# Kernel optimization log

Hardware: AMD Instinct MI355X
Metric: run time of the kernel (lower is better)

## Reference

```python
import jax, jax.numpy as jnp
import numpy as np

B, S, HID = 2, 1024, 2048
NH, NKV = 32, 8
HD = HID // NH          # 64
N_REP = NH // NKV       # 4
ROPE_BASE = 10000.0


def rope_tables(seq_len, dim):
    inv_freq = 1.0 / (ROPE_BASE ** (np.arange(0, dim, 2, dtype=np.float32) / dim))
    t = jnp.arange(seq_len, dtype=jnp.float32)
    freqs = jnp.outer(t, jnp.asarray(inv_freq))          # [S, HD/2]
    emb = jnp.concatenate([freqs, freqs], axis=-1)       # [S, HD]
    return jnp.cos(emb), jnp.sin(emb)


def rotate_half(x):
    half = x.shape[-1] // 2
    return jnp.concatenate([-x[..., half:], x[..., :half]], axis=-1)


def setup_inputs() -> dict:
    key = jax.random.key(0)
    k1, k2, k3, k4, k5 = jax.random.split(key, 5)
    hidden_states = jax.random.normal(k1, (B, S, HID), dtype=jnp.float32)
    position_ids = jnp.broadcast_to(jnp.arange(S, dtype=jnp.int32), (B, S))
    # additive causal mask [B,1,S,S]: 0 where allowed, large negative where masked
    neg = jnp.finfo(jnp.float32).min
    causal = jnp.tril(jnp.ones((S, S), dtype=bool))
    attention_mask = jnp.where(causal, 0.0, neg)[None, None].astype(jnp.float32)
    attention_mask = jnp.broadcast_to(attention_mask, (B, 1, S, S))
    scale = 0.02
    Wq = jax.random.normal(k2, (HID, NH * HD), dtype=jnp.float32) * scale
    Wk = jax.random.normal(k3, (HID, NKV * HD), dtype=jnp.float32) * scale
    Wv = jax.random.normal(k4, (HID, NKV * HD), dtype=jnp.float32) * scale
    Wo = jax.random.normal(k5, (HID, HID), dtype=jnp.float32) * scale
    return {"hidden_states": hidden_states, "position_ids": position_ids,
            "attention_mask": attention_mask, "Wq": Wq, "Wk": Wk, "Wv": Wv, "Wo": Wo}


def reference(hidden_states, position_ids, attention_mask, Wq, Wk, Wv, Wo):
    b, s, _ = hidden_states.shape
    q = (hidden_states @ Wq).reshape(b, s, NH, HD).transpose(0, 2, 1, 3)    # [b,H,s,d]
    k = (hidden_states @ Wk).reshape(b, s, NKV, HD).transpose(0, 2, 1, 3)   # [b,kv,s,d]
    v = (hidden_states @ Wv).reshape(b, s, NKV, HD).transpose(0, 2, 1, 3)

    cos_t, sin_t = rope_tables(s, HD)                    # [s, d]
    cos = cos_t[position_ids][:, None]                   # [b,1,s,d]
    sin = sin_t[position_ids][:, None]
    q = q * cos + rotate_half(q) * sin
    k = k * cos + rotate_half(k) * sin

    # GQA: repeat each kv head N_REP times along the head axis
    k = jnp.repeat(k, N_REP, axis=1)                     # [b,H,s,d]
    v = jnp.repeat(v, N_REP, axis=1)

    scale = 1.0 / jnp.sqrt(jnp.asarray(HD, dtype=q.dtype))
    scores = jnp.einsum('bhqd,bhkd->bhqk', q, k) * scale
    scores = scores + attention_mask
    scores = jnp.maximum(scores, jnp.finfo(scores.dtype).min)
    w = jax.nn.softmax(scores, axis=-1)
    out = jnp.einsum('bhqk,bhkd->bhqd', w, v)            # [b,H,s,d]
    out = out.transpose(0, 2, 1, 3).reshape(b, s, HID)
    return out @ Wo
```

## Files before the change

### kernel.cpp

```cpp
#include <hip/hip_runtime.h>
#include <hip/hip_bf16.h>
#include <math.h>

constexpr int BB   = 2;
constexpr int SS   = 1024;
constexpr int HID  = 2048;
constexpr int NH   = 32;
constexpr int NKV  = 8;
constexpr int HD   = 64;
constexpr int M    = BB * SS;
constexpr int NQKV = 3072;

typedef __attribute__((ext_vector_type(8))) short bf8v;
typedef __attribute__((ext_vector_type(4))) float f4v;

static __device__ __forceinline__ unsigned short f2b(float x) {
  __hip_bfloat16 h = __float2bfloat16(x);
  return *reinterpret_cast<unsigned short*>(&h);
}
static __device__ __forceinline__ void gload16(void* lds, const void* g) {
  __builtin_amdgcn_global_load_lds(
      (const __attribute__((address_space(1))) void*)g,
      (__attribute__((address_space(3))) void*)lds, 16, 0, 0);
}

__global__ __launch_bounds__(256) void prepAll(
    const float* __restrict__ Wq, const float* __restrict__ Wk,
    const float* __restrict__ Wv, const float* __restrict__ Wo,
    const float* __restrict__ hidden, const int* __restrict__ pos_ids,
    unsigned short* __restrict__ WqkvT, unsigned short* __restrict__ WoT,
    unsigned short* __restrict__ Xb, float2* __restrict__ tab) {
  const int z = blockIdx.z;
  const int t = threadIdx.x;

  if (z == 4) {
    const int idx = blockIdx.y * 32 + blockIdx.x;
    if ((t & 127) < 32) {
      const int m = idx * 2 + (t >> 7);
      const int j = t & 31;
      const float pos = (float)pos_ids[m];
      const float ang = pos * exp2f(-(float)j * (13.287712379549449f / 32.0f));
      float sn, cs;
      sincosf(ang, &sn, &cs);
      tab[(size_t)m * 32 + j] = make_float2(cs, sn);
    }
    return;
  }
  if (z == 5) {
    const size_t base = ((size_t)(blockIdx.y * 32 + blockIdx.x)) * 4096;
#pragma unroll
    for (int it = 0; it < 2; ++it) {
      const size_t i = base + it * 2048 + t * 8;
      const float4 v0 = *(const float4*)(hidden + i);
      const float4 v1 = *(const float4*)(hidden + i + 4);
      unsigned short o[8] = {f2b(v0.x), f2b(v0.y), f2b(v0.z), f2b(v0.w),
                             f2b(v1.x), f2b(v1.y), f2b(v1.z), f2b(v1.w)};
      *(bf8v*)(Xb + i) = *(bf8v*)o;
    }
    return;
  }

  const float* src;
  unsigned short* dst;
  int C;
  if (z == 0)      { src = Wq; dst = WqkvT;                      C = 2048; }
  else if (z == 1) { src = Wk; dst = WqkvT + (size_t)2048 * HID; C = 512;  }
  else if (z == 2) { src = Wv; dst = WqkvT + (size_t)2560 * HID; C = 512;  }
  else             { src = Wo; dst = WoT;                        C = 2048; }

  const int r0 = blockIdx.y * 64, c0 = blockIdx.x * 64;
  if (c0 >= C) return;
  __shared__ float T[64][65];
  {
    const int r  = t >> 2;
    const int c4 = (t & 3) * 16;
    const float* sp = src + (size_t)(r0 + r) * C + c0 + c4;
    *(float4*)&T[r][c4 + 0]  = *(const float4*)(sp + 0);
    *(float4*)&T[r][c4 + 4]  = *(const float4*)(sp + 4);
    *(float4*)&T[r][c4 + 8]  = *(const float4*)(sp + 8);
    *(float4*)&T[r][c4 + 12] = *(const float4*)(sp + 12);
  }
  __syncthreads();
  {
    const int c  = t >> 2;
    const int rr = (t & 3) * 16;
    unsigned short o[16];
#pragma unroll
    for (int i = 0; i < 16; ++i) o[i] = f2b(T[rr + i][c]);
    unsigned short* dp = dst + (size_t)(c0 + c) * HID + r0 + rr;
    *(bf8v*)dp       = *(bf8v*)&o[0];
    *(bf8v*)(dp + 8) = *(bf8v*)&o[8];
  }
}


__global__ __launch_bounds__(256) void gemm_qkv(
    const unsigned short* __restrict__ A, const unsigned short* __restrict__ Bt,
    const float2* __restrict__ tab,
    unsigned short* __restrict__ Qb, unsigned short* __restrict__ Kb,
    unsigned short* __restrict__ Vb) {
  __shared__ unsigned short As[4][64 * 32];
  __shared__ unsigned short Bs[4][128 * 32];
  const int t  = threadIdx.x;
  const int w  = t >> 6, l = t & 63;
  const int lr = l & 15, lg = l >> 4;
  const int wr = w >> 1, wc = w & 1;
  const int bm = blockIdx.y * 64, bn = blockIdx.x * 128;

  f4v acc[2][4] = {};

  const unsigned short* Ablk = A  + (size_t)bm * HID;
  const unsigned short* Bblk = Bt + (size_t)bn * HID;
  const int srow = l >> 2;
  const int scol = (((l & 3) ^ ((srow >> 1) & 3)) * 8);
  const int rsl  = (lg ^ ((lr >> 1) & 3)) * 8;

  auto stage = [&](int buf, int k0) {
    gload16(&As[buf][(w * 16) * 32], Ablk + (size_t)(w * 16 + srow) * HID + k0 + scol);
    gload16(&Bs[buf][(w * 32)      * 32], Bblk + (size_t)(w * 32 +      srow) * HID + k0 + scol);
    gload16(&Bs[buf][(w * 32 + 16) * 32], Bblk + (size_t)(w * 32 + 16 + srow) * HID + k0 + scol);
  };

  const int nsteps = HID / 32;
  stage(0, 0);
  stage(1, 32);
  stage(2, 64);
  asm volatile("s_waitcnt vmcnt(6)" ::: "memory");
  __builtin_amdgcn_s_barrier();

  const int aoff = (wr * 32 + lr) * 32 + rsl;
  const int boff = (wc * 64 + lr) * 32 + rsl;
  for (int tt = 0; tt < nsteps; ++tt) {
    const int cur = tt & 3;
    if (tt + 3 < nsteps) stage((tt + 3) & 3, (tt + 3) * 32);

    bf8v aF[2], bF[4];
#pragma unroll
    for (int i = 0; i < 2; ++i)
      aF[i] = *(const bf8v*)&As[cur][aoff + i * 512];
#pragma unroll
    for (int j = 0; j < 4; ++j)
      bF[j] = *(const bf8v*)&Bs[cur][boff + j * 512];
    __builtin_amdgcn_s_setprio(1);
#pragma unroll
    for (int mi = 0; mi < 2; ++mi)
#pragma unroll
      for (int ni = 0; ni < 4; ++ni)
        acc[mi][ni] = __builtin_amdgcn_mfma_f32_16x16x32_bf16(aF[mi], bF[ni], acc[mi][ni], 0, 0, 0);
    __builtin_amdgcn_s_setprio(0);

    if (tt + 3 < nsteps)      { asm volatile("s_waitcnt vmcnt(6)" ::: "memory"); }
    else if (tt + 2 < nsteps) { asm volatile("s_waitcnt vmcnt(3)" ::: "memory"); }
    else                      { asm volatile("s_waitcnt vmcnt(0)" ::: "memory"); }
    __builtin_amdgcn_s_barrier();
  }

  const int row0 = bm + wr * 32;
  const int colHead = bn + wc * 64;
  unsigned short* outArr;
  int hh, headsPerB, mode;
  if (colHead < 2048)      { mode = 0; outArr = Qb; hh = colHead >> 6;          headsPerB = NH;  }
  else if (colHead < 2560) { mode = 1; outArr = Kb; hh = (colHead - 2048) >> 6; headsPerB = NKV; }
  else                     { mode = 2; outArr = Vb; hh = (colHead - 2560) >> 6; headsPerB = NKV; }

#pragma unroll
  for (int mi = 0; mi < 2; ++mi)
#pragma unroll
    for (int r = 0; r < 4; ++r) {
      const int rowg = row0 + mi * 16 + lg * 4 + r;
      const int bI = rowg >> 10, s = rowg & (SS - 1);
      unsigned short* dst =
          outArr + ((size_t)(bI * headsPerB + hh) * SS + s) * 64;
      if (mode == 2) {
#pragma unroll
        for (int ni = 0; ni < 4; ++ni)
          dst[ni * 16 + lr] = f2b(acc[mi][ni][r]);
      } else {
        const float2 cs_lo = tab[(size_t)rowg * 32 + lr];
        const float2 cs_hi = tab[(size_t)rowg * 32 + 16 + lr];
#pragma unroll
        for (int ni = 0; ni < 4; ++ni) {
          const float2 cs = (ni & 1) ? cs_hi : cs_lo;
          const float x   = acc[mi][ni][r];
          const float prt = acc[mi][ni ^ 2][r];
          const float rh  = (ni < 2) ? -prt : prt;
          float v = x * cs.x + rh * cs.y;
          if (mode == 0) v *= 0.125f;
          dst[ni * 16 + lr] = f2b(v);
        }
      }
    }
}

__global__ __launch_bounds__(256) void gemm_bf16(
    const unsigned short* __restrict__ A, const unsigned short* __restrict__ Bt,
    float* __restrict__ C, int Ndim) {
  __shared__ unsigned short As[4][64 * 32];
  __shared__ unsigned short Bs[4][128 * 32];
  const int t  = threadIdx.x;
  const int w  = t >> 6, l = t & 63;
  const int lr = l & 15, lg = l >> 4;
  const int wr = w >> 1, wc = w & 1;
  const int bm = blockIdx.y * 64, bn = blockIdx.x * 128;

  f4v acc[2][4] = {};

  const unsigned short* Ablk = A  + (size_t)bm * HID;
  const unsigned short* Bblk = Bt + (size_t)bn * HID;
  const int srow = l >> 2;
  const int scol = (((l & 3) ^ ((srow >> 1) & 3)) * 8);
  const int rsl  = (lg ^ ((lr >> 1) & 3)) * 8;

  auto stage = [&](int buf, int k0) {
    gload16(&As[buf][(w * 16) * 32], Ablk + (size_t)(w * 16 + srow) * HID + k0 + scol);
    gload16(&Bs[buf][(w * 32)      * 32], Bblk + (size_t)(w * 32 +      srow) * HID + k0 + scol);
    gload16(&Bs[buf][(w * 32 + 16) * 32], Bblk + (size_t)(w * 32 + 16 + srow) * HID + k0 + scol);
  };

  const int nsteps = HID / 32;
  stage(0, 0);
  stage(1, 32);
  stage(2, 64);
  asm volatile("s_waitcnt vmcnt(6)" ::: "memory");
  __builtin_amdgcn_s_barrier();

  const int aoff = (wr * 32 + lr) * 32 + rsl;
  const int boff = (wc * 64 + lr) * 32 + rsl;
  for (int tt = 0; tt < nsteps; ++tt) {
    const int cur = tt & 3;
    if (tt + 3 < nsteps) stage((tt + 3) & 3, (tt + 3) * 32);

    bf8v aF[2], bF[4];
#pragma unroll
    for (int i = 0; i < 2; ++i)
      aF[i] = *(const bf8v*)&As[cur][aoff + i * 512];
#pragma unroll
    for (int j = 0; j < 4; ++j)
      bF[j] = *(const bf8v*)&Bs[cur][boff + j * 512];
    __builtin_amdgcn_s_setprio(1);
#pragma unroll
    for (int mi = 0; mi < 2; ++mi)
#pragma unroll
      for (int ni = 0; ni < 4; ++ni)
        acc[mi][ni] = __builtin_amdgcn_mfma_f32_16x16x32_bf16(aF[mi], bF[ni], acc[mi][ni], 0, 0, 0);
    __builtin_amdgcn_s_setprio(0);

    if (tt + 3 < nsteps)      { asm volatile("s_waitcnt vmcnt(6)" ::: "memory"); }
    else if (tt + 2 < nsteps) { asm volatile("s_waitcnt vmcnt(3)" ::: "memory"); }
    else                      { asm volatile("s_waitcnt vmcnt(0)" ::: "memory"); }
    __builtin_amdgcn_s_barrier();
  }

  const int row0 = bm + wr * 32;
  const int col0 = bn + wc * 64;
#pragma unroll
  for (int mi = 0; mi < 2; ++mi)
#pragma unroll
    for (int r = 0; r < 4; ++r) {
      const size_t rowoff = (size_t)(row0 + mi * 16 + lg * 4 + r) * Ndim;
#pragma unroll
      for (int ni = 0; ni < 4; ++ni)
        C[rowoff + col0 + ni * 16 + lr] = acc[mi][ni][r];
    }
}

__global__ __launch_bounds__(256) void vtrans(
    const unsigned short* __restrict__ Vb, unsigned short* __restrict__ Vt) {
  const int bkv = blockIdx.y;
  const int s0  = blockIdx.x * 64;
  __shared__ unsigned short T[64][72];
  const int t = threadIdx.x;
  const unsigned short* src = Vb + ((size_t)bkv * SS + s0) * 64;
  {
    const int r  = t >> 2;
    const int co = (t & 3) * 16;
    *(bf8v*)&T[r][co]     = *(const bf8v*)(src + (size_t)r * 64 + co);
    *(bf8v*)&T[r][co + 8] = *(const bf8v*)(src + (size_t)r * 64 + co + 8);
  }
  __syncthreads();
  {
    const int d  = t >> 2;
    const int so = (t & 3) * 16;
    unsigned short tmp[16];
#pragma unroll
    for (int i = 0; i < 16; ++i) tmp[i] = T[so + i][d];
    unsigned short* dst = Vt + ((size_t)(bkv * 64 + d)) * SS + s0 + so;
    *(bf8v*)dst       = *(bf8v*)&tmp[0];
    *(bf8v*)(dst + 8) = *(bf8v*)&tmp[8];
  }
}

__global__ __launch_bounds__(128) void attn_mfma(
    const unsigned short* __restrict__ Qb, const unsigned short* __restrict__ Kb,
    const unsigned short* __restrict__ Vt, unsigned short* __restrict__ attn) {
  const int xb = blockIdx.x;
  const int h = blockIdx.y, b = blockIdx.z;
  const int kv = h >> 2;
  const int w  = threadIdx.x >> 6;
  const int l  = threadIdx.x & 63;
  const int lr = l & 15;
  const int lg = l >> 4;
  const int t  = threadIdx.x;

  __shared__ unsigned short VT[64][72];
  __shared__ unsigned short PL[2][16][72];

  const unsigned short* Kp = Kb + ((size_t)((b * NKV + kv) * SS)) * 64;
  const unsigned short* Vp = Vt + ((size_t)((b * NKV + kv) * 64)) * SS;

  const int vd  = t >> 1;
  const int vso = (t & 1) * 32;

  for (int half = 0; half < 2; ++half) {
    const int qt = half ? (31 - xb) : xb;
    const int qbase = qt * 32;
    const int qW = qbase + w * 16;
    const unsigned short* Qp = Qb + ((size_t)((b * NH + h) * SS + qW)) * 64;
    bf8v aQ0 = *(const bf8v*)(Qp + (size_t)lr * 64 + lg * 8);
    bf8v aQ1 = *(const bf8v*)(Qp + (size_t)lr * 64 + 32 + lg * 8);

    f4v o[4] = {{0,0,0,0},{0,0,0,0},{0,0,0,0},{0,0,0,0}};
    float lsumL[4] = {0.f, 0.f, 0.f, 0.f};

    for (int kvb = 0; kvb < qbase + 32; kvb += 64) {
      __syncthreads();
      const unsigned short* vp = Vp + (size_t)vd * SS + kvb + vso;
      const bf8v v0 = *(const bf8v*)(vp);
      const bf8v v1 = *(const bf8v*)(vp + 8);
      const bf8v v2 = *(const bf8v*)(vp + 16);
      const bf8v v3 = *(const bf8v*)(vp + 24);

      f4v sc[4] = {{0,0,0,0},{0,0,0,0},{0,0,0,0},{0,0,0,0}};
      __builtin_amdgcn_s_setprio(1);
#pragma unroll
      for (int c = 0; c < 4; ++c) {
        const unsigned short* kr = Kp + (size_t)(kvb + c * 16 + lr) * 64 + lg * 8;
        bf8v b0 = *(const bf8v*)(kr);
        bf8v b1 = *(const bf8v*)(kr + 32);
        sc[c] = __builtin_amdgcn_mfma_f32_16x16x32_bf16(aQ0, b0, sc[c], 0, 0, 0);
        sc[c] = __builtin_amdgcn_mfma_f32_16x16x32_bf16(aQ1, b1, sc[c], 0, 0, 0);
      }
      __builtin_amdgcn_s_setprio(0);

#pragma unroll
      for (int r = 0; r < 4; ++r) {
        const int qrow = qW + lg * 4 + r;
        float ps = 0.f;
        unsigned short pb[4];
#pragma unroll
        for (int c = 0; c < 4; ++c) {
          const float s = ((kvb + c * 16 + lr) > qrow) ? -INFINITY : sc[c][r];
          const float p = __expf(s);
          ps += p;
          pb[c] = f2b(p);
        }
        lsumL[r] += ps;
#pragma unroll
        for (int c = 0; c < 4; ++c) PL[w][lg * 4 + r][c * 16 + lr] = pb[c];
      }

      *(bf8v*)&VT[vd][vso]      = v0;
      *(bf8v*)&VT[vd][vso + 8]  = v1;
      *(bf8v*)&VT[vd][vso + 16] = v2;
      *(bf8v*)&VT[vd][vso + 24] = v3;

      __syncthreads();

      bf8v aP0 = *(const bf8v*)&PL[w][lr][lg * 8];
      bf8v aP1 = *(const bf8v*)&PL[w][lr][32 + lg * 8];
      __builtin_amdgcn_s_setprio(1);
#pragma unroll
      for (int n = 0; n < 4; ++n) {
        bf8v bV0 = *(const bf8v*)&VT[n * 16 + lr][lg * 8];
        bf8v bV1 = *(const bf8v*)&VT[n * 16 + lr][32 + lg * 8];
        o[n] = __builtin_amdgcn_mfma_f32_16x16x32_bf16(aP0, bV0, o[n], 0, 0, 0);
        o[n] = __builtin_amdgcn_mfma_f32_16x16x32_bf16(aP1, bV1, o[n], 0, 0, 0);
      }
      __builtin_amdgcn_s_setprio(0);
    }

#pragma unroll
    for (int r = 0; r < 4; ++r) {
      float ls = lsumL[r];
      ls += __shfl_xor(ls, 1);
      ls += __shfl_xor(ls, 2);
      ls += __shfl_xor(ls, 4);
      ls += __shfl_xor(ls, 8);
      const float inv = 1.0f / ls;
      const int row = qW + lg * 4 + r;
      unsigned short* dst = attn + (size_t)(b * SS + row) * HID + h * 64;
#pragma unroll
      for (int n = 0; n < 4; ++n) dst[n * 16 + lr] = f2b(o[n][r] * inv);
    }
  }
}

extern "C" void kernel_launch(void* const* d_in, const int* in_sizes, int n_in,
                              void* d_out, int out_size, void* d_ws, size_t ws_size,
                              hipStream_t stream) {
  const float* hidden = (const float*)d_in[0];
  const int*   pos    = (const int*)d_in[1];
  const float* Wq = (const float*)d_in[3];
  const float* Wk = (const float*)d_in[4];
  const float* Wv = (const float*)d_in[5];
  const float* Wo = (const float*)d_in[6];
  float* out = (float*)d_out;

  char* ws = (char*)d_ws;
  unsigned short* WqkvT = (unsigned short*)(ws);
  unsigned short* WoT   = (unsigned short*)(ws + 12582912);
  unsigned short* Xb    = (unsigned short*)(ws + 20971520);
  unsigned short* attnb = Xb;
  unsigned short* Qb    = (unsigned short*)(ws + 29360128);
  unsigned short* Kb    = (unsigned short*)(ws + 37748736);
  unsigned short* Vb    = (unsigned short*)(ws + 39845888);
  unsigned short* Vt    = (unsigned short*)(ws + 41943040);
  float2*         tab   = (float2*)(ws + 44040192);

  dim3 blk(256);

  prepAll<<<dim3(32, 32, 6), blk, 0, stream>>>(Wq, Wk, Wv, Wo, hidden, pos,
                                               WqkvT, WoT, Xb, tab);

  gemm_qkv<<<dim3(NQKV / 128, M / 64), blk, 0, stream>>>(Xb, WqkvT, tab, Qb, Kb, Vb);

  vtrans<<<dim3(SS / 64, BB * NKV), blk, 0, stream>>>(Vb, Vt);

  attn_mfma<<<dim3(16, NH, BB), dim3(128), 0, stream>>>(Qb, Kb, Vt, attnb);

  gemm_bf16<<<dim3(HID / 128, M / 64), blk, 0, stream>>>(attnb, WoT, out, HID);
}
```

Measured before the change: 156.5 us.

## Double-buffer V tiles in attention and swizzle GEMM block order for XCD locality

The attention kernel now keeps two V tile buffers in LDS and prefetches the next V tile while the current one is used, so one barrier per iteration is enough instead of two. Both GEMMs switch to a 1D grid whose block index is remapped so that consecutive blocks (which AMD dispatches round-robin across XCDs) group N and M tiles, aiming for better L2 reuse per XCD. The cost is extra LDS in attention and a more complex index mapping that depends on specific grid sizes.

```diff
diff --git a/kernel.cpp b/kernel.cpp
--- a/kernel.cpp
+++ b/kernel.cpp
@@ -105,7 +105,10 @@
   const int w  = t >> 6, l = t & 63;
   const int lr = l & 15, lg = l >> 4;
   const int wr = w >> 1, wc = w & 1;
-  const int bm = blockIdx.y * 64, bn = blockIdx.x * 128;
+  const int L = blockIdx.x;
+  const int g = L & 7, s5 = L >> 3;
+  const int bn = (g * 3 + (s5 % 3)) * 128;
+  const int bm = (s5 / 3) * 64;
 
   f4v acc[2][4] = {};
 
@@ -201,7 +204,10 @@
   const int w  = t >> 6, l = t & 63;
   const int lr = l & 15, lg = l >> 4;
   const int wr = w >> 1, wc = w & 1;
-  const int bm = blockIdx.y * 64, bn = blockIdx.x * 128;
+  const int L = blockIdx.x;
+  const int g = L & 7, s5 = L >> 3;
+  const int bn = (g * 2 + (s5 & 1)) * 128;
+  const int bm = (s5 >> 1) * 64;
 
   f4v acc[2][4] = {};
 
@@ -302,7 +308,7 @@
   const int lg = l >> 4;
   const int t  = threadIdx.x;
 
-  __shared__ unsigned short VT[64][72];
+  __shared__ unsigned short VT[2][64][72];
   __shared__ unsigned short PL[2][16][72];
 
   const unsigned short* Kp = Kb + ((size_t)((b * NKV + kv) * SS)) * 64;
@@ -322,13 +328,30 @@
     f4v o[4] = {{0,0,0,0},{0,0,0,0},{0,0,0,0},{0,0,0,0}};
     float lsumL[4] = {0.f, 0.f, 0.f, 0.f};
 
-    for (int kvb = 0; kvb < qbase + 32; kvb += 64) {
-      __syncthreads();
-      const unsigned short* vp = Vp + (size_t)vd * SS + kvb + vso;
-      const bf8v v0 = *(const bf8v*)(vp);
-      const bf8v v1 = *(const bf8v*)(vp + 8);
-      const bf8v v2 = *(const bf8v*)(vp + 16);
-      const bf8v v3 = *(const bf8v*)(vp + 24);
+    const int nkv = (qbase + 32 + 63) >> 6;
+
+    {
+      const unsigned short* vp = Vp + (size_t)vd * SS + vso;
+      *(bf8v*)&VT[0][vd][vso]      = *(const bf8v*)(vp);
+      *(bf8v*)&VT[0][vd][vso + 8]  = *(const bf8v*)(vp + 8);
+      *(bf8v*)&VT[0][vd][vso + 16] = *(const bf8v*)(vp + 16);
+      *(bf8v*)&VT[0][vd][vso + 24] = *(const bf8v*)(vp + 24);
+    }
+    __syncthreads();
+
+    int cur = 0;
+    for (int it = 0; it < nkv; ++it) {
+      const int kvb = it * 64;
+      const bool hasNext = (it + 1 < nkv);
+
+      bf8v nv0, nv1, nv2, nv3;
+      if (hasNext) {
+        const unsigned short* vp = Vp + (size_t)vd * SS + kvb + 64 + vso;
+        nv0 = *(const bf8v*)(vp);
+        nv1 = *(const bf8v*)(vp + 8);
+        nv2 = *(const bf8v*)(vp + 16);
+        nv3 = *(const bf8v*)(vp + 24);
+      }
 
       f4v sc[4] = {{0,0,0,0},{0,0,0,0},{0,0,0,0},{0,0,0,0}};
       __builtin_amdgcn_s_setprio(1);
@@ -359,24 +382,27 @@
         for (int c = 0; c < 4; ++c) PL[w][lg * 4 + r][c * 16 + lr] = pb[c];
       }
 
-      *(bf8v*)&VT[vd][vso]      = v0;
-      *(bf8v*)&VT[vd][vso + 8]  = v1;
-      *(bf8v*)&VT[vd][vso + 16] = v2;
-      *(bf8v*)&VT[vd][vso + 24] = v3;
-
-      __syncthreads();
+      if (hasNext) {
+        *(bf8v*)&VT[cur ^ 1][vd][vso]      = nv0;
+        *(bf8v*)&VT[cur ^ 1][vd][vso + 8]  = nv1;
+        *(bf8v*)&VT[cur ^ 1][vd][vso + 16] = nv2;
+        *(bf8v*)&VT[cur ^ 1][vd][vso + 24] = nv3;
+      }
 
       bf8v aP0 = *(const bf8v*)&PL[w][lr][lg * 8];
       bf8v aP1 = *(const bf8v*)&PL[w][lr][32 + lg * 8];
       __builtin_amdgcn_s_setprio(1);
 #pragma unroll
       for (int n = 0; n < 4; ++n) {
-        bf8v bV0 = *(const bf8v*)&VT[n * 16 + lr][lg * 8];
-        bf8v bV1 = *(const bf8v*)&VT[n * 16 + lr][32 + lg * 8];
+        bf8v bV0 = *(const bf8v*)&VT[cur][n * 16 + lr][lg * 8];
+        bf8v bV1 = *(const bf8v*)&VT[cur][n * 16 + lr][32 + lg * 8];
         o[n] = __builtin_amdgcn_mfma_f32_16x16x32_bf16(aP0, bV0, o[n], 0, 0, 0);
         o[n] = __builtin_amdgcn_mfma_f32_16x16x32_bf16(aP1, bV1, o[n], 0, 0, 0);
       }
       __builtin_amdgcn_s_setprio(0);
+
+      __syncthreads();
+      cur ^= 1;
     }
 
 #pragma unroll
@@ -422,11 +448,11 @@
   prepAll<<<dim3(32, 32, 6), blk, 0, stream>>>(Wq, Wk, Wv, Wo, hidden, pos,
                                                WqkvT, WoT, Xb, tab);
 
-  gemm_qkv<<<dim3(NQKV / 128, M / 64), blk, 0, stream>>>(Xb, WqkvT, tab, Qb, Kb, Vb);
+  gemm_qkv<<<dim3(768), blk, 0, stream>>>(Xb, WqkvT, tab, Qb, Kb, Vb);
 
   vtrans<<<dim3(SS / 64, BB * NKV), blk, 0, stream>>>(Vb, Vt);
 
   attn_mfma<<<dim3(16, NH, BB), dim3(128), 0, stream>>>(Qb, Kb, Vt, attnb);
 
-  gemm_bf16<<<dim3(HID / 128, M / 64), blk, 0, stream>>>(attnb, WoT, out, HID);
-}
+  gemm_bf16<<<dim3(512), blk, 0, stream>>>(attnb, WoT, out, HID);
+}
```

Measured after the change: 157.8 us. No clear change (+0.8%).

## Enlarge GEMM tiles to 128x128 and remap block indices for L2 locality

Applied to the files above, without the earlier changes.

Both the QKV and output-projection GEMMs move from 64x128 to 128x128 output tiles. Each wave now computes 4x4 MFMA accumulators instead of 2x4, and the A stage loads double, so the vmcnt thresholds are adjusted to match. A 1D grid with a custom mapping spreads the column tiles of each row group across groups of 8 blocks to improve cache reuse. This raises arithmetic intensity per LDS and global byte, but it also increases register and LDS use and halves the number of blocks, which can lower occupancy and wave parallelism.

```diff
diff --git a/kernel.cpp b/kernel.cpp
--- a/kernel.cpp
+++ b/kernel.cpp
@@ -99,15 +99,18 @@
     const float2* __restrict__ tab,
     unsigned short* __restrict__ Qb, unsigned short* __restrict__ Kb,
     unsigned short* __restrict__ Vb) {
-  __shared__ unsigned short As[4][64 * 32];
+  __shared__ unsigned short As[4][128 * 32];
   __shared__ unsigned short Bs[4][128 * 32];
   const int t  = threadIdx.x;
   const int w  = t >> 6, l = t & 63;
   const int lr = l & 15, lg = l >> 4;
   const int wr = w >> 1, wc = w & 1;
-  const int bm = blockIdx.y * 64, bn = blockIdx.x * 128;
-
-  f4v acc[2][4] = {};
+  const int L = blockIdx.x;
+  const int g = L & 7, s5 = L >> 3;
+  const int bn = (g * 3 + (s5 % 3)) * 128;
+  const int bm = (s5 / 3) * 128;
+
+  f4v acc[4][4] = {};
 
   const unsigned short* Ablk = A  + (size_t)bm * HID;
   const unsigned short* Bblk = Bt + (size_t)bn * HID;
@@ -116,7 +119,8 @@
   const int rsl  = (lg ^ ((lr >> 1) & 3)) * 8;
 
   auto stage = [&](int buf, int k0) {
-    gload16(&As[buf][(w * 16) * 32], Ablk + (size_t)(w * 16 + srow) * HID + k0 + scol);
+    gload16(&As[buf][(w * 32)      * 32], Ablk + (size_t)(w * 32 +      srow) * HID + k0 + scol);
+    gload16(&As[buf][(w * 32 + 16) * 32], Ablk + (size_t)(w * 32 + 16 + srow) * HID + k0 + scol);
     gload16(&Bs[buf][(w * 32)      * 32], Bblk + (size_t)(w * 32 +      srow) * HID + k0 + scol);
     gload16(&Bs[buf][(w * 32 + 16) * 32], Bblk + (size_t)(w * 32 + 16 + srow) * HID + k0 + scol);
   };
@@ -125,37 +129,36 @@
   stage(0, 0);
   stage(1, 32);
   stage(2, 64);
-  asm volatile("s_waitcnt vmcnt(6)" ::: "memory");
+  asm volatile("s_waitcnt vmcnt(8)" ::: "memory");
   __builtin_amdgcn_s_barrier();
 
-  const int aoff = (wr * 32 + lr) * 32 + rsl;
+  const int aoff = (wr * 64 + lr) * 32 + rsl;
   const int boff = (wc * 64 + lr) * 32 + rsl;
   for (int tt = 0; tt < nsteps; ++tt) {
     const int cur = tt & 3;
     if (tt + 3 < nsteps) stage((tt + 3) & 3, (tt + 3) * 32);
 
-    bf8v aF[2], bF[4];
-#pragma unroll
-    for (int i = 0; i < 2; ++i)
+    bf8v aF[4], bF[4];
+#pragma unroll
+    for (int i = 0; i < 4; ++i) {
       aF[i] = *(const bf8v*)&As[cur][aoff + i * 512];
-#pragma unroll
-    for (int j = 0; j < 4; ++j)
-      bF[j] = *(const bf8v*)&Bs[cur][boff + j * 512];
+      bF[i] = *(const bf8v*)&Bs[cur][boff + i * 512];
+    }
     __builtin_amdgcn_s_setprio(1);
 #pragma unroll
-    for (int mi = 0; mi < 2; ++mi)
+    for (int mi = 0; mi < 4; ++mi)
 #pragma unroll
       for (int ni = 0; ni < 4; ++ni)
         acc[mi][ni] = __builtin_amdgcn_mfma_f32_16x16x32_bf16(aF[mi], bF[ni], acc[mi][ni], 0, 0, 0);
     __builtin_amdgcn_s_setprio(0);
 
-    if (tt + 3 < nsteps)      { asm volatile("s_waitcnt vmcnt(6)" ::: "memory"); }
-    else if (tt + 2 < nsteps) { asm volatile("s_waitcnt vmcnt(3)" ::: "memory"); }
+    if (tt + 3 < nsteps)      { asm volatile("s_waitcnt vmcnt(8)" ::: "memory"); }
+    else if (tt + 2 < nsteps) { asm volatile("s_waitcnt vmcnt(4)" ::: "memory"); }
     else                      { asm volatile("s_waitcnt vmcnt(0)" ::: "memory"); }
     __builtin_amdgcn_s_barrier();
   }
 
-  const int row0 = bm + wr * 32;
+  const int row0 = bm + wr * 64;
   const int colHead = bn + wc * 64;
   unsigned short* outArr;
   int hh, headsPerB, mode;
@@ -164,7 +167,7 @@
   else                     { mode = 2; outArr = Vb; hh = (colHead - 2560) >> 6; headsPerB = NKV; }
 
 #pragma unroll
-  for (int mi = 0; mi < 2; ++mi)
+  for (int mi = 0; mi < 4; ++mi)
 #pragma unroll
     for (int r = 0; r < 4; ++r) {
       const int rowg = row0 + mi * 16 + lg * 4 + r;
@@ -195,15 +198,18 @@
 __global__ __launch_bounds__(256) void gemm_bf16(
     const unsigned short* __restrict__ A, const unsigned short* __restrict__ Bt,
     float* __restrict__ C, int Ndim) {
-  __shared__ unsigned short As[4][64 * 32];
+  __shared__ unsigned short As[4][128 * 32];
   __shared__ unsigned short Bs[4][128 * 32];
   const int t  = threadIdx.x;
   const int w  = t >> 6, l = t & 63;
   const int lr = l & 15, lg = l >> 4;
   const int wr = w >> 1, wc = w & 1;
-  const int bm = blockIdx.y * 64, bn = blockIdx.x * 128;
-
-  f4v acc[2][4] = {};
+  const int L = blockIdx.x;
+  const int g = L & 7, s5 = L >> 3;
+  const int bn = (g * 2 + (s5 & 1)) * 128;
+  const int bm = (s5 >> 1) * 128;
+
+  f4v acc[4][4] = {};
 
   const unsigned short* Ablk = A  + (size_t)bm * HID;
   const unsigned short* Bblk = Bt + (size_t)bn * HID;
@@ -212,7 +218,8 @@
   const int rsl  = (lg ^ ((lr >> 1) & 3)) * 8;
 
   auto stage = [&](int buf, int k0) {
-    gload16(&As[buf][(w * 16) * 32], Ablk + (size_t)(w * 16 + srow) * HID + k0 + scol);
+    gload16(&As[buf][(w * 32)      * 32], Ablk + (size_t)(w * 32 +      srow) * HID + k0 + scol);
+    gload16(&As[buf][(w * 32 + 16) * 32], Ablk + (size_t)(w * 32 + 16 + srow) * HID + k0 + scol);
     gload16(&Bs[buf][(w * 32)      * 32], Bblk + (size_t)(w * 32 +      srow) * HID + k0 + scol);
     gload16(&Bs[buf][(w * 32 + 16) * 32], Bblk + (size_t)(w * 32 + 16 + srow) * HID + k0 + scol);
   };
@@ -221,40 +228,39 @@
   stage(0, 0);
   stage(1, 32);
   stage(2, 64);
-  asm volatile("s_waitcnt vmcnt(6)" ::: "memory");
+  asm volatile("s_waitcnt vmcnt(8)" ::: "memory");
   __builtin_amdgcn_s_barrier();
 
-  const int aoff = (wr * 32 + lr) * 32 + rsl;
+  const int aoff = (wr * 64 + lr) * 32 + rsl;
   const int boff = (wc * 64 + lr) * 32 + rsl;
   for (int tt = 0; tt < nsteps; ++tt) {
     const int cur = tt & 3;
     if (tt + 3 < nsteps) stage((tt + 3) & 3, (tt + 3) * 32);
 
-    bf8v aF[2], bF[4];
-#pragma unroll
-    for (int i = 0; i < 2; ++i)
+    bf8v aF[4], bF[4];
+#pragma unroll
+    for (int i = 0; i < 4; ++i) {
       aF[i] = *(const bf8v*)&As[cur][aoff + i * 512];
-#pragma unroll
-    for (int j = 0; j < 4; ++j)
-      bF[j] = *(const bf8v*)&Bs[cur][boff + j * 512];
+      bF[i] = *(const bf8v*)&Bs[cur][boff + i * 512];
+    }
     __builtin_amdgcn_s_setprio(1);
 #pragma unroll
-    for (int mi = 0; mi < 2; ++mi)
+    for (int mi = 0; mi < 4; ++mi)
 #pragma unroll
       for (int ni = 0; ni < 4; ++ni)
         acc[mi][ni] = __builtin_amdgcn_mfma_f32_16x16x32_bf16(aF[mi], bF[ni], acc[mi][ni], 0, 0, 0);
     __builtin_amdgcn_s_setprio(0);
 
-    if (tt + 3 < nsteps)      { asm volatile("s_waitcnt vmcnt(6)" ::: "memory"); }
-    else if (tt + 2 < nsteps) { asm volatile("s_waitcnt vmcnt(3)" ::: "memory"); }
+    if (tt + 3 < nsteps)      { asm volatile("s_waitcnt vmcnt(8)" ::: "memory"); }
+    else if (tt + 2 < nsteps) { asm volatile("s_waitcnt vmcnt(4)" ::: "memory"); }
     else                      { asm volatile("s_waitcnt vmcnt(0)" ::: "memory"); }
     __builtin_amdgcn_s_barrier();
   }
 
-  const int row0 = bm + wr * 32;
+  const int row0 = bm + wr * 64;
   const int col0 = bn + wc * 64;
 #pragma unroll
-  for (int mi = 0; mi < 2; ++mi)
+  for (int mi = 0; mi < 4; ++mi)
 #pragma unroll
     for (int r = 0; r < 4; ++r) {
       const size_t rowoff = (size_t)(row0 + mi * 16 + lg * 4 + r) * Ndim;
@@ -422,11 +428,11 @@
   prepAll<<<dim3(32, 32, 6), blk, 0, stream>>>(Wq, Wk, Wv, Wo, hidden, pos,
                                                WqkvT, WoT, Xb, tab);
 
-  gemm_qkv<<<dim3(NQKV / 128, M / 64), blk, 0, stream>>>(Xb, WqkvT, tab, Qb, Kb, Vb);
+  gemm_qkv<<<dim3(384), blk, 0, stream>>>(Xb, WqkvT, tab, Qb, Kb, Vb);
 
   vtrans<<<dim3(SS / 64, BB * NKV), blk, 0, stream>>>(Vb, Vt);
 
   attn_mfma<<<dim3(16, NH, BB), dim3(128), 0, stream>>>(Qb, Kb, Vt, attnb);
 
-  gemm_bf16<<<dim3(HID / 128, M / 64), blk, 0, stream>>>(attnb, WoT, out, HID);
-}
+  gemm_bf16<<<dim3(256), blk, 0, stream>>>(attnb, WoT, out, HID);
+}
```

After: 174.3 us. +11.4%, slower.
